# Optimization experiments

Measured on AMD Instinct MI355X. Metric: run time of the kernel, lower is better.

The kernel has to match this reference:

```python
import math
import jax, jax.numpy as jnp
import numpy as np

D = 2048
N = 16
B = 2
L = 4096
SCALE = math.sqrt(1.0 / float(N))


def setup_inputs() -> dict:
    key = jax.random.key(0)
    ks = jax.random.split(key, 6)
    x = jax.random.normal(ks[0], (B, D, L), dtype=jnp.float32)
    alpha = 0.2 * jax.random.normal(ks[1], (D, N, 1), dtype=jnp.float32)
    delta = 0.2 * jax.random.normal(ks[2], (D, N, 1), dtype=jnp.float32)
    theta = 0.2 * jax.random.normal(ks[3], (D, 1, 1), dtype=jnp.float32)
    gamma = jax.random.normal(ks[4], (D, N, 2), dtype=jnp.float32)
    omega = jax.random.normal(ks[5], (D,), dtype=jnp.float32)
    return {"x": x, "alpha": alpha, "delta": delta, "theta": theta,
            "gamma": gamma, "omega": omega}


def _coeffs(alpha, delta, theta, gamma):
    p = jax.nn.sigmoid(alpha)                       # (D, N, 1)
    d = jax.nn.sigmoid(delta)                       # (D, N, 1)
    wave = jnp.arange(1, N + 1, dtype=jnp.float32).reshape(1, N, 1)
    base = jax.nn.sigmoid(theta) * (2.0 * math.pi / float(N))  # (D,1,1)
    phi = wave * base                               # (D, N, 1)
    q = (1.0 - p * d).astype(jnp.complex64) * jnp.exp(1j * phi)  # (D, N, 1)
    gam = (gamma[..., 0] + 1j * gamma[..., 1]) * SCALE            # (D, N)
    return p, q, gam


def _fftconv_real(x, k):
    # x: (B, D, L), k: (D, L)  -> causal conv, keep first L samples
    n = L + L - 1
    n_fft = 1 << (n - 1).bit_length()
    X = jnp.fft.rfft(x, n=n_fft)                    # (B, D, n_fft//2+1)
    K = jnp.fft.rfft(k, n=n_fft)[None]              # (1, D, n_fft//2+1)
    y = jnp.fft.irfft(X * K, n=n_fft)[..., :L]
    return y.astype(x.dtype)


def reference(x, alpha, delta, theta, gamma, omega):
    p, q, gam = _coeffs(alpha, delta, theta, gamma)
    # kernel_d[t] = Re( sum_n p_dn * gamma_dn * q_dn^t )
    t = jnp.arange(L, dtype=jnp.float32)
    V = jnp.exp(t[None, None, :] * jnp.log(q))      # (D, N, L) = q^t
    kernel = jnp.real(jnp.sum(p * gam[..., None] * V, axis=1))  # (D, L)
    y = _fftconv_real(x, kernel) + x * omega[None, :, None]
    # last state: h_t = q * h_{t-1} + p * x_t  (hx = None)
    qs = q[..., 0]                                   # (D, N)
    ps = p[..., 0]                                   # (D, N)
    xs = jnp.moveaxis(x, -1, 0)                      # (L, B, D)
    h0 = jnp.zeros((B, D, N), dtype=jnp.complex64)

    def step(h, xt):
        # xt: (B, D); px_t = p_dn * x_t[b,d]
        h = qs[None] * h + ps[None] * xt[..., None].astype(jnp.complex64)
        return h, None

    h_last, _ = jax.lax.scan(step, h0, xs)
    h_ri = jnp.stack([h_last.real, h_last.imag], axis=-1)  # (B, D, N, 2)
    return y, h_ri
```

## Files before the change

kernel.cpp:

```cpp
#include <hip/hip_runtime.h>
#include <math.h>


constexpr int kD = 2048, kN = 16, kB = 2, kL = 4096;
constexpr int kT  = 128;
constexpr int kCH = kL / kT;
constexpr float kSCALE = 0.25f;

typedef float v2 __attribute__((ext_vector_type(2)));

static __device__ __forceinline__ v2 mkv2(float a, float b) {
    v2 r; r.x = a; r.y = b; return r;
}

static __device__ __forceinline__ v2 v2fma(v2 a, v2 b, v2 c) {
#if __has_builtin(__builtin_elementwise_fma)
    return __builtin_elementwise_fma(a, b, c);
#else
    v2 r;
    r.x = __builtin_fmaf(a.x, b.x, c.x);
    r.y = __builtin_fmaf(a.y, b.y, c.y);
    return r;
#endif
}

__global__ __launch_bounds__(kT, 2) void fused_kernel(
    const float* __restrict__ x,     const float* __restrict__ alpha,
    const float* __restrict__ delta, const float* __restrict__ theta,
    const float* __restrict__ gamma, const float* __restrict__ omega,
    float* __restrict__ y,           float* __restrict__ hout)
{
    __shared__ float cqr[kN], cqi[kN], cgr[kN], cgi[kN], cp[kN];
    __shared__ float pubr[kN], pubi[kN];

    const int row   = blockIdx.x;
    const int d     = row & (kD - 1);
    const int tid   = threadIdx.x;
    const int llane = tid & 63;

    const float4* xp = (const float4*)(x + (size_t)row * kL + (size_t)tid * kCH);

    float xs[kCH];
    {
        float4 tb[8];
#pragma unroll
        for (int k = 0; k < 8; k++) tb[k] = xp[k];
#pragma unroll
        for (int k = 0; k < 8; k++) {
            xs[4*k+0] = tb[k].x; xs[4*k+1] = tb[k].y;
            xs[4*k+2] = tb[k].z; xs[4*k+3] = tb[k].w;
        }
    }

    if (tid < kN) {
        int n = tid, i = d * kN + n;
        float p  = 1.0f / (1.0f + expf(-alpha[i]));
        float dd = 1.0f / (1.0f + expf(-delta[i]));
        float th = 1.0f / (1.0f + expf(-theta[d]));
        float phi = (float)(n + 1) * th * 0.39269908169872414f;
        float r = 1.0f - p * dd;
        float s, c;
        sincosf(phi, &s, &c);
        cqr[n] = r * c;
        cqi[n] = r * s;
        cgr[n] = p * kSCALE * gamma[2 * i];
        cgi[n] = -(p * kSCALE * gamma[2 * i + 1]);
        cp[n]  = p;
    }
    __syncthreads();

    v2 u[kN];
    {
        v2 qx[kN], qy[kN];
#pragma unroll
        for (int n = 0; n < kN; n++) {
            qx[n] = mkv2(cqr[n],  cqr[n]);
            qy[n] = mkv2(-cqi[n], cqi[n]);
        }
#pragma unroll
        for (int n = 0; n < kN; n++) u[n] = mkv2(xs[0], 0.0f);
#pragma unroll
        for (int j = 1; j < kCH; j++) {
            v2 xv = mkv2(xs[j], 0.0f);
#pragma unroll
            for (int n = 0; n < kN; n++) {
                v2 a = v2fma(qx[n], u[n], xv);
                u[n] = v2fma(qy[n], mkv2(u[n].y, u[n].x), a);
            }
        }
    }

    v2 m[kN];
#pragma unroll
    for (int n = 0; n < kN; n++) m[n] = mkv2(cqr[n], cqi[n]);
#pragma unroll
    for (int k = 0; k < 5; k++) {
#pragma unroll
        for (int n = 0; n < kN; n++) {
            float mr = m[n].x, mi = m[n].y;
            m[n] = mkv2(__builtin_fmaf(mr, mr, -(mi * mi)), 2.0f * mr * mi);
        }
    }

    const bool w1 = (tid >= 64);
    v2 W[kN];
#pragma unroll
    for (int n = 0; n < kN; n++) W[n] = m[n];
#pragma unroll
    for (int k = 0; k < 6; k++) {
        const int s = 1 << k;
#pragma unroll
        for (int n = 0; n < kN; n++) {
            float tr = __shfl_up(u[n].x, (unsigned)s, 64);
            float ti = __shfl_up(u[n].y, (unsigned)s, 64);
            if (llane >= s) {
                u[n].x = __builtin_fmaf(m[n].x, tr,
                          __builtin_fmaf(-m[n].y, ti, u[n].x));
                u[n].y = __builtin_fmaf(m[n].x, ti,
                          __builtin_fmaf( m[n].y, tr, u[n].y));
            }
        }
        if (w1 && (llane & s)) {
#pragma unroll
            for (int n = 0; n < kN; n++) {
                float wr = W[n].x, wi = W[n].y;
                W[n].x = __builtin_fmaf(wr, m[n].x, -(wi * m[n].y));
                W[n].y = __builtin_fmaf(wr, m[n].y,  wi * m[n].x);
            }
        }
        if (k < 5) {
#pragma unroll
            for (int n = 0; n < kN; n++) {
                float mr = m[n].x, mi = m[n].y;
                m[n] = mkv2(__builtin_fmaf(mr, mr, -(mi * mi)), 2.0f * mr * mi);
            }
        }
    }

    float4 tb[8];
#pragma unroll
    for (int k = 0; k < 8; k++) tb[k] = xp[k];

    if (tid == 63) {
#pragma unroll
        for (int n = 0; n < kN; n++) { pubr[n] = u[n].x; pubi[n] = u[n].y; }
    }
    __syncthreads();
    if (w1) {
#pragma unroll
        for (int n = 0; n < kN; n++) {
            float pr = pubr[n], pi = pubi[n];
            u[n].x = __builtin_fmaf(W[n].x, pr,
                      __builtin_fmaf(-W[n].y, pi, u[n].x));
            u[n].y = __builtin_fmaf(W[n].x, pi,
                      __builtin_fmaf( W[n].y, pr, u[n].y));
        }
    }

    if (tid == kT - 1) {
        float4* hp = (float4*)(hout + (size_t)row * (kN * 2));
#pragma unroll
        for (int n = 0; n < kN; n += 2)
            hp[n >> 1] = make_float4(cp[n] * u[n].x,         cp[n] * u[n].y,
                                     cp[n + 1] * u[n + 1].x, cp[n + 1] * u[n + 1].y);
    }

#pragma unroll
    for (int n = 0; n < kN; n++) {
        float pr = __shfl_up(u[n].x, 1, 64);
        float pi = __shfl_up(u[n].y, 1, 64);
        u[n] = mkv2(pr, pi);
    }
    if (llane == 0) {
#pragma unroll
        for (int n = 0; n < kN; n++)
            u[n] = (tid == 0) ? mkv2(0.0f, 0.0f) : mkv2(pubr[n], pubi[n]);
    }

#pragma unroll
    for (int k = 0; k < 8; k++) {
        xs[4*k+0] = tb[k].x; xs[4*k+1] = tb[k].y;
        xs[4*k+2] = tb[k].z; xs[4*k+3] = tb[k].w;
    }

    v2 qx[kN], qy[kN], g[kN];
#pragma unroll
    for (int n = 0; n < kN; n++) {
        qx[n] = mkv2(cqr[n],  cqr[n]);
        qy[n] = mkv2(-cqi[n], cqi[n]);
        g[n]  = mkv2(cgr[n],  cgi[n]);
    }
    const float om = omega[d];

    float ys[kCH];
#pragma unroll
    for (int j = 0; j < kCH; j++) {
        float xj = xs[j];
        v2 xv = mkv2(xj, 0.0f);
        v2 acc0 = mkv2(0.0f, 0.0f), acc1 = mkv2(0.0f, 0.0f);
        v2 acc2 = mkv2(0.0f, 0.0f), acc3 = mkv2(0.0f, 0.0f);
#pragma unroll
        for (int n = 0; n < kN; n += 4) {
            v2 a;
            a = v2fma(qx[n],   u[n],   xv);
            u[n]   = v2fma(qy[n],   mkv2(u[n].y,   u[n].x),   a);
            acc0   = v2fma(g[n],    u[n],   acc0);
            a = v2fma(qx[n+1], u[n+1], xv);
            u[n+1] = v2fma(qy[n+1], mkv2(u[n+1].y, u[n+1].x), a);
            acc1   = v2fma(g[n+1],  u[n+1], acc1);
            a = v2fma(qx[n+2], u[n+2], xv);
            u[n+2] = v2fma(qy[n+2], mkv2(u[n+2].y, u[n+2].x), a);
            acc2   = v2fma(g[n+2],  u[n+2], acc2);
            a = v2fma(qx[n+3], u[n+3], xv);
            u[n+3] = v2fma(qy[n+3], mkv2(u[n+3].y, u[n+3].x), a);
            acc3   = v2fma(g[n+3],  u[n+3], acc3);
        }
        v2 s = (acc0 + acc1) + (acc2 + acc3);
        ys[j] = s.x + s.y + om * xj;
    }

    float4* yp = (float4*)(y + (size_t)row * kL + (size_t)tid * kCH);
#pragma unroll
    for (int k = 0; k < 8; k++)
        yp[k] = make_float4(ys[4*k+0], ys[4*k+1], ys[4*k+2], ys[4*k+3]);
}

extern "C" void kernel_launch(void* const* d_in, const int* in_sizes, int n_in,
                              void* d_out, int out_size, void* d_ws, size_t ws_size,
                              hipStream_t stream) {
    const float* x     = (const float*)d_in[0];
    const float* alpha = (const float*)d_in[1];
    const float* delta = (const float*)d_in[2];
    const float* theta = (const float*)d_in[3];
    const float* gamma = (const float*)d_in[4];
    const float* omega = (const float*)d_in[5];
    float* y    = (float*)d_out;
    float* hout = y + (size_t)kB * kD * kL;

    fused_kernel<<<kB * kD, kT, 0, stream>>>(x, alpha, delta, theta, gamma,
                                             omega, y, hout);
}
```

Baseline: 186.8 us.

## Use real second-order recurrence per mode and process four rows per block

Each complex first-order recurrence h = q*h + x is replaced with an equivalent real second-order recurrence s_t = 2a*s_{t-1} - |q|^2*s_{t-2} + x_t. Output and state are rebuilt from (s, s_prev) with precomputed coefficients, and scan-combine matrices come from repeated doubling. This about halves per-step FMA work compared with the packed complex update. Each block also loops over four rows, using double-buffered shared coefficients and prefetching the next row's x, which cuts the grid size by four and amortises setup. The cost is more serial work per block and possible numerical differences from the second-order form.

```diff
diff --git a/kernel.cpp b/kernel.cpp
--- a/kernel.cpp
+++ b/kernel.cpp
@@ -3,26 +3,11 @@
 
 
 constexpr int kD = 2048, kN = 16, kB = 2, kL = 4096;
-constexpr int kT  = 128;
-constexpr int kCH = kL / kT;
+constexpr int kT   = 128;
+constexpr int kCH  = kL / kT;
+constexpr int kRPB = 4;
+constexpr int kGrid = (kB * kD) / kRPB;
 constexpr float kSCALE = 0.25f;
-
-typedef float v2 __attribute__((ext_vector_type(2)));
-
-static __device__ __forceinline__ v2 mkv2(float a, float b) {
-    v2 r; r.x = a; r.y = b; return r;
-}
-
-static __device__ __forceinline__ v2 v2fma(v2 a, v2 b, v2 c) {
-#if __has_builtin(__builtin_elementwise_fma)
-    return __builtin_elementwise_fma(a, b, c);
-#else
-    v2 r;
-    r.x = __builtin_fmaf(a.x, b.x, c.x);
-    r.y = __builtin_fmaf(a.y, b.y, c.y);
-    return r;
-#endif
-}
 
 __global__ __launch_bounds__(kT, 2) void fused_kernel(
     const float* __restrict__ x,     const float* __restrict__ alpha,
@@ -30,199 +15,237 @@
     const float* __restrict__ gamma, const float* __restrict__ omega,
     float* __restrict__ y,           float* __restrict__ hout)
 {
-    __shared__ float cqr[kN], cqi[kN], cgr[kN], cgi[kN], cp[kN];
-    __shared__ float pubr[kN], pubi[kN];
-
-    const int row   = blockIdx.x;
-    const int d     = row & (kD - 1);
+    __shared__ float c2a[2][kN], ccc[2][kN], caa[2][kN], cbb[2][kN];
+    __shared__ float cc1[2][kN], cc2[2][kN], cpr[2][kN];
+    __shared__ float pubs[2][kN], pubp[2][kN];
+
     const int tid   = threadIdx.x;
     const int llane = tid & 63;
-
-    const float4* xp = (const float4*)(x + (size_t)row * kL + (size_t)tid * kCH);
-
-    float xs[kCH];
+    const bool w1   = (tid >= 64);
+    const int row0  = blockIdx.x * kRPB;
+
+    float4 tb[8];
     {
-        float4 tb[8];
+        const float4* xp = (const float4*)(x + (size_t)row0 * kL + (size_t)tid * kCH);
 #pragma unroll
         for (int k = 0; k < 8; k++) tb[k] = xp[k];
+    }
+
+#pragma unroll 1
+    for (int r = 0; r < kRPB; ++r) {
+        const int row = row0 + r;
+        const int d   = row & (kD - 1);
+        const int pp  = r & 1;
+
+        if (tid < kN) {
+            int n = tid, i = d * kN + n;
+            float p  = 1.0f / (1.0f + expf(-alpha[i]));
+            float dd = 1.0f / (1.0f + expf(-delta[i]));
+            float th = 1.0f / (1.0f + expf(-theta[d]));
+            float phi = (float)(n + 1) * th * 0.39269908169872414f;
+            float rr = 1.0f - p * dd;
+            float sn, cs;
+            sincosf(phi, &sn, &cs);
+            float a = rr * cs, b = rr * sn;
+            float gr = p * kSCALE * gamma[2 * i];
+            float gi = -(p * kSCALE * gamma[2 * i + 1]);
+            c2a[pp][n] = a + a;
+            ccc[pp][n] = __builtin_fmaf(a, a, b * b);
+            caa[pp][n] = a;
+            cbb[pp][n] = b;
+            cc1[pp][n] = gr;
+            cc2[pp][n] = __builtin_fmaf(gi, b, -(gr * a));
+            cpr[pp][n] = p;
+        }
+
+        float xs[kCH];
 #pragma unroll
         for (int k = 0; k < 8; k++) {
             xs[4*k+0] = tb[k].x; xs[4*k+1] = tb[k].y;
             xs[4*k+2] = tb[k].z; xs[4*k+3] = tb[k].w;
         }
+        __syncthreads();
+
+        float twoa[kN], cc[kN];
+#pragma unroll
+        for (int n = 0; n < kN; n++) { twoa[n] = c2a[pp][n]; cc[n] = ccc[pp][n]; }
+
+        float ss[kN], sq[kN];
+#pragma unroll
+        for (int n = 0; n < kN; n++) { ss[n] = xs[0]; sq[n] = 0.0f; }
+#pragma unroll
+        for (int j = 1; j < kCH; j++) {
+            float xj = xs[j];
+#pragma unroll
+            for (int n = 0; n < kN; n++) {
+                float t  = __builtin_fmaf(-cc[n], sq[n], xj);
+                float sn = __builtin_fmaf(twoa[n], ss[n], t);
+                sq[n] = ss[n];
+                ss[n] = sn;
+            }
+        }
+
+        float al[kN], be[kN];
+        {
+            float aa[kN];
+#pragma unroll
+            for (int n = 0; n < kN; n++) {
+                aa[n] = caa[pp][n];
+                al[n] = twoa[n];
+                be[n] = 1.0f;
+            }
+#pragma unroll
+            for (int sdb = 0; sdb < 4; sdb++) {
+#pragma unroll
+                for (int n = 0; n < kN; n++) {
+                    float t  = __builtin_fmaf(-cc[n], be[n], aa[n] * al[n]);
+                    float nb = __builtin_fmaf(-cc[n], be[n] * be[n], al[n] * al[n]);
+                    al[n] = (al[n] + al[n]) * t;
+                    be[n] = nb;
+                }
+            }
+        }
+
+        float Wa[kN], Wb[kN];
+#pragma unroll
+        for (int n = 0; n < kN; n++) { Wa[n] = al[n]; Wb[n] = be[n]; }
+#pragma unroll
+        for (int rd = 0; rd < 6; rd++) {
+            const int sh = 1 << rd;
+#pragma unroll
+            for (int n = 0; n < kN; n++) {
+                float cb  = cc[n] * be[n];
+                float e00 = __builtin_fmaf(twoa[n], al[n], -cb);
+                float e01 = -(cc[n] * al[n]);
+                float ts  = __shfl_up(ss[n], (unsigned)sh, 64);
+                float tp  = __shfl_up(sq[n], (unsigned)sh, 64);
+                if (llane >= sh) {
+                    ss[n] = __builtin_fmaf(e00, ts,
+                            __builtin_fmaf(e01, tp, ss[n]));
+                    sq[n] = __builtin_fmaf(al[n], ts,
+                            __builtin_fmaf(-cb, tp, sq[n]));
+                }
+            }
+            if (w1 && (llane & sh)) {
+#pragma unroll
+                for (int n = 0; n < kN; n++) {
+                    float t1 = Wa[n] * al[n];
+                    float t2 = Wb[n] * be[n];
+                    float t3 = __builtin_fmaf(Wa[n], be[n], al[n] * Wb[n]);
+                    Wa[n] = __builtin_fmaf(twoa[n], t1, -(cc[n] * t3));
+                    Wb[n] = __builtin_fmaf(-cc[n], t2, t1);
+                }
+            }
+            if (rd < 5) {
+#pragma unroll
+                for (int n = 0; n < kN; n++) {
+                    float t  = __builtin_fmaf(-cc[n], be[n],
+                               0.5f * (twoa[n] * al[n]));
+                    float nb = __builtin_fmaf(-cc[n], be[n] * be[n],
+                                              al[n] * al[n]);
+                    al[n] = (al[n] + al[n]) * t;
+                    be[n] = nb;
+                }
+            }
+        }
+
+        if (tid == 63) {
+#pragma unroll
+            for (int n = 0; n < kN; n++) { pubs[pp][n] = ss[n]; pubp[pp][n] = sq[n]; }
+        }
+        __syncthreads();
+        if (w1) {
+#pragma unroll
+            for (int n = 0; n < kN; n++) {
+                float cb  = cc[n] * Wb[n];
+                float e00 = __builtin_fmaf(twoa[n], Wa[n], -cb);
+                float e01 = -(cc[n] * Wa[n]);
+                float ps  = pubs[pp][n], pq = pubp[pp][n];
+                ss[n] = __builtin_fmaf(e00, ps,
+                        __builtin_fmaf(e01, pq, ss[n]));
+                sq[n] = __builtin_fmaf(Wa[n], ps,
+                        __builtin_fmaf(-cb, pq, sq[n]));
+            }
+        }
+
+        if (tid == kT - 1) {
+            float4* hp = (float4*)(hout + (size_t)row * (kN * 2));
+#pragma unroll
+            for (int k = 0; k < kN / 2; k++) {
+                int n0 = 2 * k, n1 = 2 * k + 1;
+                float hr0 = cpr[pp][n0] *
+                            __builtin_fmaf(-caa[pp][n0], sq[n0], ss[n0]);
+                float hi0 = cpr[pp][n0] * cbb[pp][n0] * sq[n0];
+                float hr1 = cpr[pp][n1] *
+                            __builtin_fmaf(-caa[pp][n1], sq[n1], ss[n1]);
+                float hi1 = cpr[pp][n1] * cbb[pp][n1] * sq[n1];
+                hp[k] = make_float4(hr0, hi0, hr1, hi1);
+            }
+        }
+
+#pragma unroll
+        for (int n = 0; n < kN; n++) {
+            float ts = __shfl_up(ss[n], 1, 64);
+            float tp = __shfl_up(sq[n], 1, 64);
+            ss[n] = ts; sq[n] = tp;
+        }
+        if (llane == 0) {
+#pragma unroll
+            for (int n = 0; n < kN; n++) {
+                ss[n] = (tid == 0) ? 0.0f : pubs[pp][n];
+                sq[n] = (tid == 0) ? 0.0f : pubp[pp][n];
+            }
+        }
+
+        if (r + 1 < kRPB) {
+            const float4* xn = (const float4*)(x + (size_t)(row + 1) * kL +
+                                               (size_t)tid * kCH);
+#pragma unroll
+            for (int k = 0; k < 8; k++) tb[k] = xn[k];
+        }
+
+        float c1[kN], c2[kN];
+#pragma unroll
+        for (int n = 0; n < kN; n++) { c1[n] = cc1[pp][n]; c2[n] = cc2[pp][n]; }
+        const float om = omega[d];
+
+        float ys[kCH];
+#pragma unroll
+        for (int j = 0; j < kCH; j++) {
+            float xj = xs[j];
+            float acc0 = om * xj, acc1 = 0.0f, acc2 = 0.0f, acc3 = 0.0f;
+#pragma unroll
+            for (int n = 0; n < kN; n += 4) {
+                float t, sn;
+                t  = __builtin_fmaf(-cc[n],   sq[n],   xj);
+                sn = __builtin_fmaf(twoa[n],  ss[n],   t);
+                acc0 = __builtin_fmaf(c1[n],   sn,     acc0);
+                acc0 = __builtin_fmaf(c2[n],   ss[n],  acc0);
+                sq[n] = ss[n]; ss[n] = sn;
+                t  = __builtin_fmaf(-cc[n+1], sq[n+1], xj);
+                sn = __builtin_fmaf(twoa[n+1], ss[n+1], t);
+                acc1 = __builtin_fmaf(c1[n+1], sn,     acc1);
+                acc1 = __builtin_fmaf(c2[n+1], ss[n+1], acc1);
+                sq[n+1] = ss[n+1]; ss[n+1] = sn;
+                t  = __builtin_fmaf(-cc[n+2], sq[n+2], xj);
+                sn = __builtin_fmaf(twoa[n+2], ss[n+2], t);
+                acc2 = __builtin_fmaf(c1[n+2], sn,     acc2);
+                acc2 = __builtin_fmaf(c2[n+2], ss[n+2], acc2);
+                sq[n+2] = ss[n+2]; ss[n+2] = sn;
+                t  = __builtin_fmaf(-cc[n+3], sq[n+3], xj);
+                sn = __builtin_fmaf(twoa[n+3], ss[n+3], t);
+                acc3 = __builtin_fmaf(c1[n+3], sn,     acc3);
+                acc3 = __builtin_fmaf(c2[n+3], ss[n+3], acc3);
+                sq[n+3] = ss[n+3]; ss[n+3] = sn;
+            }
+            ys[j] = (acc0 + acc1) + (acc2 + acc3);
+        }
+
+        float4* yp = (float4*)(y + (size_t)row * kL + (size_t)tid * kCH);
+#pragma unroll
+        for (int k = 0; k < 8; k++)
+            yp[k] = make_float4(ys[4*k+0], ys[4*k+1], ys[4*k+2], ys[4*k+3]);
     }
-
-    if (tid < kN) {
-        int n = tid, i = d * kN + n;
-        float p  = 1.0f / (1.0f + expf(-alpha[i]));
-        float dd = 1.0f / (1.0f + expf(-delta[i]));
-        float th = 1.0f / (1.0f + expf(-theta[d]));
-        float phi = (float)(n + 1) * th * 0.39269908169872414f;
-        float r = 1.0f - p * dd;
-        float s, c;
-        sincosf(phi, &s, &c);
-        cqr[n] = r * c;
-        cqi[n] = r * s;
-        cgr[n] = p * kSCALE * gamma[2 * i];
-        cgi[n] = -(p * kSCALE * gamma[2 * i + 1]);
-        cp[n]  = p;
-    }
-    __syncthreads();
-
-    v2 u[kN];
-    {
-        v2 qx[kN], qy[kN];
-#pragma unroll
-        for (int n = 0; n < kN; n++) {
-            qx[n] = mkv2(cqr[n],  cqr[n]);
-            qy[n] = mkv2(-cqi[n], cqi[n]);
-        }
-#pragma unroll
-        for (int n = 0; n < kN; n++) u[n] = mkv2(xs[0], 0.0f);
-#pragma unroll
-        for (int j = 1; j < kCH; j++) {
-            v2 xv = mkv2(xs[j], 0.0f);
-#pragma unroll
-            for (int n = 0; n < kN; n++) {
-                v2 a = v2fma(qx[n], u[n], xv);
-                u[n] = v2fma(qy[n], mkv2(u[n].y, u[n].x), a);
-            }
-        }
-    }
-
-    v2 m[kN];
-#pragma unroll
-    for (int n = 0; n < kN; n++) m[n] = mkv2(cqr[n], cqi[n]);
-#pragma unroll
-    for (int k = 0; k < 5; k++) {
-#pragma unroll
-        for (int n = 0; n < kN; n++) {
-            float mr = m[n].x, mi = m[n].y;
-            m[n] = mkv2(__builtin_fmaf(mr, mr, -(mi * mi)), 2.0f * mr * mi);
-        }
-    }
-
-    const bool w1 = (tid >= 64);
-    v2 W[kN];
-#pragma unroll
-    for (int n = 0; n < kN; n++) W[n] = m[n];
-#pragma unroll
-    for (int k = 0; k < 6; k++) {
-        const int s = 1 << k;
-#pragma unroll
-        for (int n = 0; n < kN; n++) {
-            float tr = __shfl_up(u[n].x, (unsigned)s, 64);
-            float ti = __shfl_up(u[n].y, (unsigned)s, 64);
-            if (llane >= s) {
-                u[n].x = __builtin_fmaf(m[n].x, tr,
-                          __builtin_fmaf(-m[n].y, ti, u[n].x));
-                u[n].y = __builtin_fmaf(m[n].x, ti,
-                          __builtin_fmaf( m[n].y, tr, u[n].y));
-            }
-        }
-        if (w1 && (llane & s)) {
-#pragma unroll
-            for (int n = 0; n < kN; n++) {
-                float wr = W[n].x, wi = W[n].y;
-                W[n].x = __builtin_fmaf(wr, m[n].x, -(wi * m[n].y));
-                W[n].y = __builtin_fmaf(wr, m[n].y,  wi * m[n].x);
-            }
-        }
-        if (k < 5) {
-#pragma unroll
-            for (int n = 0; n < kN; n++) {
-                float mr = m[n].x, mi = m[n].y;
-                m[n] = mkv2(__builtin_fmaf(mr, mr, -(mi * mi)), 2.0f * mr * mi);
-            }
-        }
-    }
-
-    float4 tb[8];
-#pragma unroll
-    for (int k = 0; k < 8; k++) tb[k] = xp[k];
-
-    if (tid == 63) {
-#pragma unroll
-        for (int n = 0; n < kN; n++) { pubr[n] = u[n].x; pubi[n] = u[n].y; }
-    }
-    __syncthreads();
-    if (w1) {
-#pragma unroll
-        for (int n = 0; n < kN; n++) {
-            float pr = pubr[n], pi = pubi[n];
-            u[n].x = __builtin_fmaf(W[n].x, pr,
-                      __builtin_fmaf(-W[n].y, pi, u[n].x));
-            u[n].y = __builtin_fmaf(W[n].x, pi,
-                      __builtin_fmaf( W[n].y, pr, u[n].y));
-        }
-    }
-
-    if (tid == kT - 1) {
-        float4* hp = (float4*)(hout + (size_t)row * (kN * 2));
-#pragma unroll
-        for (int n = 0; n < kN; n += 2)
-            hp[n >> 1] = make_float4(cp[n] * u[n].x,         cp[n] * u[n].y,
-                                     cp[n + 1] * u[n + 1].x, cp[n + 1] * u[n + 1].y);
-    }
-
-#pragma unroll
-    for (int n = 0; n < kN; n++) {
-        float pr = __shfl_up(u[n].x, 1, 64);
-        float pi = __shfl_up(u[n].y, 1, 64);
-        u[n] = mkv2(pr, pi);
-    }
-    if (llane == 0) {
-#pragma unroll
-        for (int n = 0; n < kN; n++)
-            u[n] = (tid == 0) ? mkv2(0.0f, 0.0f) : mkv2(pubr[n], pubi[n]);
-    }
-
-#pragma unroll
-    for (int k = 0; k < 8; k++) {
-        xs[4*k+0] = tb[k].x; xs[4*k+1] = tb[k].y;
-        xs[4*k+2] = tb[k].z; xs[4*k+3] = tb[k].w;
-    }
-
-    v2 qx[kN], qy[kN], g[kN];
-#pragma unroll
-    for (int n = 0; n < kN; n++) {
-        qx[n] = mkv2(cqr[n],  cqr[n]);
-        qy[n] = mkv2(-cqi[n], cqi[n]);
-        g[n]  = mkv2(cgr[n],  cgi[n]);
-    }
-    const float om = omega[d];
-
-    float ys[kCH];
-#pragma unroll
-    for (int j = 0; j < kCH; j++) {
-        float xj = xs[j];
-        v2 xv = mkv2(xj, 0.0f);
-        v2 acc0 = mkv2(0.0f, 0.0f), acc1 = mkv2(0.0f, 0.0f);
-        v2 acc2 = mkv2(0.0f, 0.0f), acc3 = mkv2(0.0f, 0.0f);
-#pragma unroll
-        for (int n = 0; n < kN; n += 4) {
-            v2 a;
-            a = v2fma(qx[n],   u[n],   xv);
-            u[n]   = v2fma(qy[n],   mkv2(u[n].y,   u[n].x),   a);
-            acc0   = v2fma(g[n],    u[n],   acc0);
-            a = v2fma(qx[n+1], u[n+1], xv);
-            u[n+1] = v2fma(qy[n+1], mkv2(u[n+1].y, u[n+1].x), a);
-            acc1   = v2fma(g[n+1],  u[n+1], acc1);
-            a = v2fma(qx[n+2], u[n+2], xv);
-            u[n+2] = v2fma(qy[n+2], mkv2(u[n+2].y, u[n+2].x), a);
-            acc2   = v2fma(g[n+2],  u[n+2], acc2);
-            a = v2fma(qx[n+3], u[n+3], xv);
-            u[n+3] = v2fma(qy[n+3], mkv2(u[n+3].y, u[n+3].x), a);
-            acc3   = v2fma(g[n+3],  u[n+3], acc3);
-        }
-        v2 s = (acc0 + acc1) + (acc2 + acc3);
-        ys[j] = s.x + s.y + om * xj;
-    }
-
-    float4* yp = (float4*)(y + (size_t)row * kL + (size_t)tid * kCH);
-#pragma unroll
-    for (int k = 0; k < 8; k++)
-        yp[k] = make_float4(ys[4*k+0], ys[4*k+1], ys[4*k+2], ys[4*k+3]);
 }
 
 extern "C" void kernel_launch(void* const* d_in, const int* in_sizes, int n_in,
@@ -237,6 +260,6 @@
     float* y    = (float*)d_out;
     float* hout = y + (size_t)kB * kD * kL;
 
-    fused_kernel<<<kB * kD, kT, 0, stream>>>(x, alpha, delta, theta, gamma,
-                                             omega, y, hout);
+    fused_kernel<<<kGrid, kT, 0, stream>>>(x, alpha, delta, theta, gamma,
+                                           omega, y, hout);
 }
```

New measurement: 193.4 us. 1.04x slower.
